# Kernel tuning notes

Measured on AMD Instinct MI355X. Metric: run time of the kernel, lower is better.

The kernel has to match this reference:

```python
import jax, jax.numpy as jnp
import numpy as np

DIM = 512
NUM_EXPERTS = 8
HID = 4 * DIM
B, S = 2, 2048


def setup_inputs() -> dict:
    key = jax.random.key(0)
    ks = jax.random.split(key, 7)
    sc = 0.02
    x = jax.random.normal(ks[0], (B, S, DIM), dtype=jnp.float32)
    Wr = jax.random.normal(ks[1], (DIM, NUM_EXPERTS), dtype=jnp.float32) * sc
    br = jnp.zeros((NUM_EXPERTS,), dtype=jnp.float32)
    W1 = jax.random.normal(ks[2], (NUM_EXPERTS, DIM, HID), dtype=jnp.float32) * sc
    b1 = jnp.zeros((NUM_EXPERTS, HID), dtype=jnp.float32)
    W2 = jax.random.normal(ks[3], (NUM_EXPERTS, HID, DIM), dtype=jnp.float32) * sc
    b2 = jnp.zeros((NUM_EXPERTS, DIM), dtype=jnp.float32)
    return {"x": x, "Wr": Wr, "br": br, "W1": W1, "b1": b1, "W2": W2, "b2": b2}


def reference(x, Wr, br, W1, b1, W2, b2):
    b, s, d = x.shape
    E = Wr.shape[1]
    xf = x.reshape(-1, d)                                   # [N, d]
    N = xf.shape[0]
    logits = xf @ Wr + br                                   # [N, E]
    probs = jax.nn.softmax(logits, axis=-1)
    top_w, top_idx = jax.lax.top_k(probs, 2)                # [N, 2]
    top_w = jax.nn.softmax(top_w, axis=-1)                  # renormalize top-2
    # combine weight per (token, expert); topk indices are distinct so add is safe
    comb = jnp.zeros((N, E), dtype=xf.dtype)
    comb = comb.at[jnp.arange(N)[:, None], top_idx].add(top_w)  # [N, E]
    # dense per-expert MLP (eval mode: dropout is identity); exact GELU as nn.GELU
    h = jax.nn.gelu(jnp.einsum('nd,edf->enf', xf, W1) + b1[:, None, :], approximate=False)
    y = jnp.einsum('enf,efd->end', h, W2) + b2[:, None, :]  # [E, N, d]
    out = jnp.einsum('end,ne->nd', y, comb)                 # weighted combine
    # load-balancing loss
    load = jnp.zeros((E,), dtype=jnp.float32).at[top_idx.reshape(-1)].add(1.0)
    load = load / load.sum()
    lb_loss = jnp.sum((load - 1.0 / E) ** 2)
    return out.reshape(b, s, d), lb_loss, load
```

## Files before the change

### kernel.cpp

```cpp
#include <hip/hip_runtime.h>
#include <hip/hip_bf16.h>

#define DIMD 512
#define NEXP 8
#define HIDN 2048
#define NTOK 4096
#define NASG 8192

typedef short bf16x8 __attribute__((ext_vector_type(8)));
typedef float f32x4 __attribute__((ext_vector_type(4)));

__device__ inline unsigned short f2bf(float f) {
  __hip_bfloat16 h = __float2bfloat16(f);
  return __builtin_bit_cast(unsigned short, h);
}

__device__ inline void gl16(const void* g, void* l) {
  __builtin_amdgcn_global_load_lds(
      (const __attribute__((address_space(1))) unsigned int*)g,
      (__attribute__((address_space(3))) unsigned int*)l, 16, 0, 0);
}

__global__ __launch_bounds__(256) void transpose_both_kernel(
    const float* __restrict__ W1, const float* __restrict__ W2,
    unsigned short* __restrict__ w1t, unsigned short* __restrict__ w2t) {
  __shared__ float tile[64][65];
  int z = blockIdx.z;
  int e = z & 7;
  const float* src; unsigned short* dst; int R, C, r0, c0;
  if (z < 8) { src = W1; dst = w1t; R = DIMD; C = HIDN; c0 = blockIdx.x * 64; r0 = blockIdx.y * 64; }
  else       { src = W2; dst = w2t; R = HIDN; C = DIMD; r0 = blockIdx.x * 64; c0 = blockIdx.y * 64; }
  const float* s = src + (size_t)e * R * C;
  unsigned short* d = dst + (size_t)e * R * C;
  for (int i = threadIdx.x; i < 4096; i += 256) {
    int r = i >> 6, c = i & 63;
    tile[r][c] = s[(size_t)(r0 + r) * C + (c0 + c)];
  }
  __syncthreads();
  for (int i = threadIdx.x; i < 2048; i += 256) {
    int c = i >> 5;
    int r = (i & 31) * 2;
    unsigned lo = f2bf(tile[r][c]);
    unsigned hi = f2bf(tile[r + 1][c]);
    *reinterpret_cast<unsigned*>(d + (size_t)(c0 + c) * R + (r0 + r)) = lo | (hi << 16);
  }
}

__global__ __launch_bounds__(256) void router_kernel(const float* __restrict__ x,
                                                     const float* __restrict__ Wr,
                                                     const float* __restrict__ br,
                                                     int* __restrict__ tidx,
                                                     float* __restrict__ tw,
                                                     unsigned short* __restrict__ xb) {
  int lane = threadIdx.x & 63;
  int n = blockIdx.x * 4 + (threadIdx.x >> 6);
  const float* xr = x + (size_t)n * DIMD;
  unsigned short* xbr = xb + (size_t)n * DIMD;
  float acc[NEXP];
#pragma unroll
  for (int e = 0; e < NEXP; ++e) acc[e] = 0.f;
#pragma unroll
  for (int it = 0; it < 2; ++it) {
    int d0 = it * 256 + lane * 4;
    float4 xv = *reinterpret_cast<const float4*>(xr + d0);
    unsigned p0 = (unsigned)f2bf(xv.x) | ((unsigned)f2bf(xv.y) << 16);
    unsigned p1 = (unsigned)f2bf(xv.z) | ((unsigned)f2bf(xv.w) << 16);
    *reinterpret_cast<uint2*>(xbr + d0) = make_uint2(p0, p1);
    const float* wr = Wr + (size_t)d0 * NEXP;
#pragma unroll
    for (int j = 0; j < 4; ++j) {
      float xj = (&xv.x)[j];
#pragma unroll
      for (int e = 0; e < NEXP; ++e) acc[e] += xj * wr[j * NEXP + e];
    }
  }
#pragma unroll
  for (int e = 0; e < NEXP; ++e) {
    float v = acc[e];
#pragma unroll
    for (int off = 32; off > 0; off >>= 1) v += __shfl_xor(v, off, 64);
    acc[e] = v + br[e];
  }
  if (lane == 0) {
    float m = acc[0];
    for (int e = 1; e < NEXP; ++e) m = fmaxf(m, acc[e]);
    float p[NEXP], s = 0.f;
    for (int e = 0; e < NEXP; ++e) { p[e] = expf(acc[e] - m); s += p[e]; }
    float inv = 1.f / s;
    for (int e = 0; e < NEXP; ++e) p[e] *= inv;
    int i0 = 0; float p0 = p[0];
    for (int e = 1; e < NEXP; ++e) if (p[e] > p0) { p0 = p[e]; i0 = e; }
    int i1 = (i0 == 0) ? 1 : 0; float p1 = p[i1];
    for (int e = 0; e < NEXP; ++e) if (e != i0 && p[e] > p1) { p1 = p[e]; i1 = e; }
    float t = expf(p1 - p0);
    float w0 = 1.f / (1.f + t);
    tidx[2 * n] = i0; tidx[2 * n + 1] = i1;
    tw[2 * n] = w0; tw[2 * n + 1] = t * w0;
  }
}

__global__ __launch_bounds__(1024) void route_pack_kernel(const int* __restrict__ tidx,
                                                          int* __restrict__ off,
                                                          int* __restrict__ list,
                                                          float* __restrict__ out_tail) {
  int tid = threadIdx.x;
  int wv = tid >> 6, lane = tid & 63;

  int ids[8];
#pragma unroll
  for (int j = 0; j < 8; ++j) ids[j] = tidx[tid * 8 + j];

  int c[NEXP];
#pragma unroll
  for (int e = 0; e < NEXP; ++e) c[e] = 0;
#pragma unroll
  for (int j = 0; j < 8; ++j)
#pragma unroll
    for (int e = 0; e < NEXP; ++e) c[e] += (ids[j] == e) ? 1 : 0;

  int inc[NEXP];
#pragma unroll
  for (int e = 0; e < NEXP; ++e) {
    int v = c[e];
#pragma unroll
    for (int d = 1; d < 64; d <<= 1) {
      int t = __shfl_up(v, d, 64);
      if (lane >= d) v += t;
    }
    inc[e] = v;
  }

  __shared__ int wtot[NEXP][16];
  __shared__ int wbase[NEXP][16];
  __shared__ int ebase[NEXP];
  if (lane == 63) {
#pragma unroll
    for (int e = 0; e < NEXP; ++e) wtot[e][wv] = inc[e];
  }
  __syncthreads();
  if (tid == 0) {
    int o = 0;
    float lb = 0.f;
    for (int e = 0; e < NEXP; ++e) {
      int s = 0;
      for (int w = 0; w < 16; ++w) { wbase[e][w] = s; s += wtot[e][w]; }
      ebase[e] = o;
      off[e] = o;
      o += s;
      float l = (float)s / (float)NASG;
      out_tail[1 + e] = l;
      float dd = l - 0.125f;
      lb += dd * dd;
    }
    off[NEXP] = o;
    out_tail[0] = lb;
  }
  __syncthreads();

  int pos[NEXP];
#pragma unroll
  for (int e = 0; e < NEXP; ++e)
    pos[e] = ebase[e] + wbase[e][wv] + (inc[e] - c[e]);

#pragma unroll
  for (int j = 0; j < 8; ++j) {
    int e = ids[j];
    int p = 0;
#pragma unroll
    for (int k = 0; k < NEXP; ++k)
      if (e == k) { p = pos[k]; pos[k] = p + 1; }
    list[p] = tid * 8 + j;
  }
}


__global__ __launch_bounds__(256) void gemm1_kernel(
    const unsigned short* __restrict__ xb,
    const unsigned short* __restrict__ w1t,
    const float* __restrict__ b1,
    const int* __restrict__ off,
    const int* __restrict__ list,
    unsigned short* __restrict__ H) {
  int e = blockIdx.x;
  int offe = off[e];
  int cnt_e = off[e + 1] - offe;
  int n0 = blockIdx.y * 128;
  int m0 = blockIdx.z * 128;
  if (m0 >= cnt_e) return;

  __shared__ char ldsb[36864];

  int tid = threadIdx.x, wv = tid >> 6, lane = tid & 63;
  int rp = lane >> 3, sl = lane & 7;
  int sx = sl ^ rp;
  int rowadd = rp * 2 + (sx >> 2);
  int kq = sx & 3;

  const unsigned short* w1e = w1t + (size_t)e * HIDN * DIMD;
  const unsigned short* asrc[2];
  const unsigned short* bsrc[2];
#pragma unroll
  for (int i = 0; i < 2; ++i) {
    int r = wv * 32 + i * 16 + rowadd;
    int rr = m0 + r;
    int tok = 0;
    if (rr < cnt_e) tok = list[offe + rr] >> 1;
    asrc[i] = xb + (size_t)tok * DIMD + kq * 8;
    bsrc[i] = w1e + (size_t)(n0 + r) * DIMD + kq * 8;
  }
  int dstA0 = wv * 2048;
  int dstA1 = wv * 2048 + 1024;

  f32x4 zero = {0.f, 0.f, 0.f, 0.f};
  f32x4 acc[4][4];
#pragma unroll
  for (int m = 0; m < 4; ++m)
#pragma unroll
    for (int n = 0; n < 4; ++n) acc[m][n] = zero;

  int wave_m = wv >> 1, wave_n = wv & 1;
  int lane16 = lane & 15, kq4 = lane >> 4;
  int ra[4], rb[4];
#pragma unroll
  for (int m = 0; m < 4; ++m) {
    int r = wave_m * 64 + m * 16 + lane16;
    ra[m] = (r >> 1) * 128 + ((((kq4 + (r & 1) * 4)) ^ ((r >> 1) & 7)) << 4);
    int rn = wave_n * 64 + m * 16 + lane16;
    rb[m] = (rn >> 1) * 128 + ((((kq4 + (rn & 1) * 4)) ^ ((rn >> 1) & 7)) << 4);
  }

  const int T = DIMD / 32;
  gl16(asrc[0], ldsb + dstA0);
  gl16(asrc[1], ldsb + dstA1);
  gl16(bsrc[0], ldsb + 8192 + dstA0);
  gl16(bsrc[1], ldsb + 8192 + dstA1);
  __syncthreads();

  for (int t = 0; t < T; ++t) {
    char* cb = ldsb + (t & 1) * 16384;
    if (t + 1 < T) {
      char* nb = ldsb + ((t + 1) & 1) * 16384;
      int k0 = (t + 1) * 32;
      gl16(asrc[0] + k0, nb + dstA0);
      gl16(asrc[1] + k0, nb + dstA1);
      gl16(bsrc[0] + k0, nb + 8192 + dstA0);
      gl16(bsrc[1] + k0, nb + 8192 + dstA1);
    }
    bf16x8 af[4], bfr[4];
#pragma unroll
    for (int m = 0; m < 4; ++m) af[m] = *reinterpret_cast<const bf16x8*>(cb + ra[m]);
#pragma unroll
    for (int n = 0; n < 4; ++n) bfr[n] = *reinterpret_cast<const bf16x8*>(cb + 8192 + rb[n]);
#pragma unroll
    for (int m = 0; m < 4; ++m)
#pragma unroll
      for (int n = 0; n < 4; ++n)
        acc[m][n] = __builtin_amdgcn_mfma_f32_16x16x32_bf16(af[m], bfr[n], acc[m][n], 0, 0, 0);
    __syncthreads();
  }

  unsigned short* Ct = (unsigned short*)ldsb;
  const float* b1e = b1 + e * HIDN;
#pragma unroll
  for (int n = 0; n < 4; ++n) {
    int cl = wave_n * 64 + n * 16 + lane16;
    float bias = b1e[n0 + cl];
#pragma unroll
    for (int m = 0; m < 4; ++m) {
#pragma unroll
      for (int q = 0; q < 4; ++q) {
        int rl = wave_m * 64 + m * 16 + kq4 * 4 + q;
        float v = acc[m][n][q] + bias;
        float g = 0.5f * v * (1.f + erff(v * 0.70710678118654752f));
        Ct[rl * 136 + cl] = f2bf(g);
      }
    }
  }
  __syncthreads();
  for (int u = tid; u < 2048; u += 256) {
    int rl = u >> 4, c8 = (u & 15) * 8;
    int r = m0 + rl;
    if (r < cnt_e) {
      uint4 v = *reinterpret_cast<const uint4*>(Ct + rl * 136 + c8);
      *reinterpret_cast<uint4*>(H + (size_t)(offe + r) * HIDN + n0 + c8) = v;
    }
  }
}

__global__ __launch_bounds__(256) void gemm2_kernel(
    const unsigned short* __restrict__ H,
    const unsigned short* __restrict__ w2t,
    const float* __restrict__ b2,
    const int* __restrict__ off,
    const int* __restrict__ list,
    const float* __restrict__ tw,
    float* __restrict__ Yw) {
  int e = blockIdx.x;
  int offe = off[e];
  int cnt_e = off[e + 1] - offe;
  int n0 = blockIdx.y * 128;
  int m0 = blockIdx.z * 128;
  if (m0 >= cnt_e) return;

  __shared__ char ldsb[32768];

  int tid = threadIdx.x, wv = tid >> 6, lane = tid & 63;
  int rp = lane >> 3, sl = lane & 7;
  int sx = sl ^ rp;
  int rowadd = rp * 2 + (sx >> 2);
  int kq = sx & 3;

  const unsigned short* w2e = w2t + (size_t)e * DIMD * HIDN;
  const unsigned short* asrc[2];
  const unsigned short* bsrc[2];
#pragma unroll
  for (int i = 0; i < 2; ++i) {
    int r = wv * 32 + i * 16 + rowadd;
    int rowa = offe + m0 + r;
    if (rowa > NASG - 1) rowa = NASG - 1;
    asrc[i] = H + (size_t)rowa * HIDN + kq * 8;
    bsrc[i] = w2e + (size_t)(n0 + r) * HIDN + kq * 8;
  }
  int dstA0 = wv * 2048;
  int dstA1 = wv * 2048 + 1024;

  f32x4 zero = {0.f, 0.f, 0.f, 0.f};
  f32x4 acc[4][4];
#pragma unroll
  for (int m = 0; m < 4; ++m)
#pragma unroll
    for (int n = 0; n < 4; ++n) acc[m][n] = zero;

  int wave_m = wv >> 1, wave_n = wv & 1;
  int lane16 = lane & 15, kq4 = lane >> 4;
  int ra[4], rb[4];
#pragma unroll
  for (int m = 0; m < 4; ++m) {
    int r = wave_m * 64 + m * 16 + lane16;
    ra[m] = (r >> 1) * 128 + ((((kq4 + (r & 1) * 4)) ^ ((r >> 1) & 7)) << 4);
    int rn = wave_n * 64 + m * 16 + lane16;
    rb[m] = (rn >> 1) * 128 + ((((kq4 + (rn & 1) * 4)) ^ ((rn >> 1) & 7)) << 4);
  }

  const int T = HIDN / 32;
  gl16(asrc[0], ldsb + dstA0);
  gl16(asrc[1], ldsb + dstA1);
  gl16(bsrc[0], ldsb + 8192 + dstA0);
  gl16(bsrc[1], ldsb + 8192 + dstA1);
  __syncthreads();

  for (int t = 0; t < T; ++t) {
    char* cb = ldsb + (t & 1) * 16384;
    if (t + 1 < T) {
      char* nb = ldsb + ((t + 1) & 1) * 16384;
      int k0 = (t + 1) * 32;
      gl16(asrc[0] + k0, nb + dstA0);
      gl16(asrc[1] + k0, nb + dstA1);
      gl16(bsrc[0] + k0, nb + 8192 + dstA0);
      gl16(bsrc[1] + k0, nb + 8192 + dstA1);
    }
    bf16x8 af[4], bfr[4];
#pragma unroll
    for (int m = 0; m < 4; ++m) af[m] = *reinterpret_cast<const bf16x8*>(cb + ra[m]);
#pragma unroll
    for (int n = 0; n < 4; ++n) bfr[n] = *reinterpret_cast<const bf16x8*>(cb + 8192 + rb[n]);
#pragma unroll
    for (int m = 0; m < 4; ++m)
#pragma unroll
      for (int n = 0; n < 4; ++n)
        acc[m][n] = __builtin_amdgcn_mfma_f32_16x16x32_bf16(af[m], bfr[n], acc[m][n], 0, 0, 0);
    __syncthreads();
  }

  const float* b2e = b2 + e * DIMD;
  float bias[4];
#pragma unroll
  for (int n = 0; n < 4; ++n) bias[n] = b2e[n0 + wave_n * 64 + n * 16 + lane16];
#pragma unroll
  for (int m = 0; m < 4; ++m) {
#pragma unroll
    for (int q = 0; q < 4; ++q) {
      int r = m0 + wave_m * 64 + m * 16 + kq4 * 4 + q;
      if (r < cnt_e) {
        int a = list[offe + r];
        float w = tw[a];
        float* yrow = Yw + (size_t)a * DIMD;
#pragma unroll
        for (int n = 0; n < 4; ++n) {
          int col = n0 + wave_n * 64 + n * 16 + lane16;
          yrow[col] = w * (acc[m][n][q] + bias[n]);
        }
      }
    }
  }
}

__global__ __launch_bounds__(256) void combine_kernel(const float* __restrict__ Yw,
                                                      float* __restrict__ out) {
  int i = (blockIdx.x * 256 + threadIdx.x) * 4;
  int n = i >> 9;
  int d = i & 511;
  float4 a = *reinterpret_cast<const float4*>(Yw + (size_t)(2 * n) * DIMD + d);
  float4 b = *reinterpret_cast<const float4*>(Yw + (size_t)(2 * n + 1) * DIMD + d);
  float4 o;
  o.x = a.x + b.x; o.y = a.y + b.y; o.z = a.z + b.z; o.w = a.w + b.w;
  *reinterpret_cast<float4*>(out + i) = o;
}

extern "C" void kernel_launch(void* const* d_in, const int* in_sizes, int n_in,
                              void* d_out, int out_size, void* d_ws, size_t ws_size,
                              hipStream_t stream) {
  const float* x  = (const float*)d_in[0];
  const float* Wr = (const float*)d_in[1];
  const float* br = (const float*)d_in[2];
  const float* W1 = (const float*)d_in[3];
  const float* b1 = (const float*)d_in[4];
  const float* W2 = (const float*)d_in[5];
  const float* b2 = (const float*)d_in[6];
  float* out = (float*)d_out;

  char* ws = (char*)d_ws;
  unsigned short* xb  = (unsigned short*)ws;  ws += (size_t)NTOK * DIMD * 2;
  unsigned short* w1t = (unsigned short*)ws;  ws += (size_t)NEXP * HIDN * DIMD * 2;
  unsigned short* w2t = (unsigned short*)ws;  ws += (size_t)NEXP * DIMD * HIDN * 2;
  unsigned short* H   = (unsigned short*)ws;  ws += (size_t)NASG * HIDN * 2;
  float* Yw = (float*)ws;                     ws += (size_t)NASG * DIMD * 4;
  float* tw = (float*)ws;                     ws += (size_t)NASG * 4;
  int* tidx = (int*)ws;                       ws += (size_t)NASG * 4;
  int* list = (int*)ws;                       ws += (size_t)NASG * 4;
  int* offp = (int*)ws;

  transpose_both_kernel<<<dim3(32, 8, 16), 256, 0, stream>>>(W1, W2, w1t, w2t);
  router_kernel<<<NTOK / 4, 256, 0, stream>>>(x, Wr, br, tidx, tw, xb);
  route_pack_kernel<<<1, 1024, 0, stream>>>(tidx, offp, list, out + (size_t)NTOK * DIMD);
  gemm1_kernel<<<dim3(NEXP, HIDN / 128, NASG / 128), 256, 0, stream>>>(xb, w1t, b1, offp, list, H);
  gemm2_kernel<<<dim3(NEXP, DIMD / 128, NASG / 128), 256, 0, stream>>>(H, w2t, b2, offp, list, tw, Yw);
  combine_kernel<<<2048, 256, 0, stream>>>(Yw, out);
}
```

Before: 118.5 us.

## Keep two global-to-LDS loads in flight with vmcnt-gated barriers in expert GEMMs

Both expert GEMM main loops are rewritten so two K-stages are prefetched before the loop starts. Each iteration waits only for the older stage (s_waitcnt vmcnt(4)) before its barrier, instead of draining all memory ops through __syncthreads. The next stage is issued into the buffer just consumed, after a post-compute barrier, so one load stays outstanding during each compute step. This aims to hide global load latency better, at the cost of an extra barrier per iteration and reliance on hand-placed waitcnt and sched_barrier ordering.

```diff
diff --git a/kernel.cpp b/kernel.cpp
--- a/kernel.cpp
+++ b/kernel.cpp
@@ -20,6 +20,19 @@
       (const __attribute__((address_space(1))) unsigned int*)g,
       (__attribute__((address_space(3))) unsigned int*)l, 16, 0, 0);
 }
+
+#define PIPE_WAIT4_BAR() do { \
+  asm volatile("s_waitcnt vmcnt(4)" ::: "memory"); \
+  __builtin_amdgcn_s_barrier(); \
+  __builtin_amdgcn_sched_barrier(0); } while (0)
+#define PIPE_WAIT0_BAR() do { \
+  asm volatile("s_waitcnt vmcnt(0)" ::: "memory"); \
+  __builtin_amdgcn_s_barrier(); \
+  __builtin_amdgcn_sched_barrier(0); } while (0)
+#define PIPE_POST_BAR() do { \
+  asm volatile("" ::: "memory"); \
+  __builtin_amdgcn_sched_barrier(0); \
+  __builtin_amdgcn_s_barrier(); } while (0)
 
 __global__ __launch_bounds__(256) void transpose_both_kernel(
     const float* __restrict__ W1, const float* __restrict__ W2,
@@ -229,23 +242,13 @@
     rb[m] = (rn >> 1) * 128 + ((((kq4 + (rn & 1) * 4)) ^ ((rn >> 1) & 7)) << 4);
   }
 
-  const int T = DIMD / 32;
-  gl16(asrc[0], ldsb + dstA0);
-  gl16(asrc[1], ldsb + dstA1);
-  gl16(bsrc[0], ldsb + 8192 + dstA0);
-  gl16(bsrc[1], ldsb + 8192 + dstA1);
-  __syncthreads();
-
-  for (int t = 0; t < T; ++t) {
-    char* cb = ldsb + (t & 1) * 16384;
-    if (t + 1 < T) {
-      char* nb = ldsb + ((t + 1) & 1) * 16384;
-      int k0 = (t + 1) * 32;
-      gl16(asrc[0] + k0, nb + dstA0);
-      gl16(asrc[1] + k0, nb + dstA1);
-      gl16(bsrc[0] + k0, nb + 8192 + dstA0);
-      gl16(bsrc[1] + k0, nb + 8192 + dstA1);
-    }
+  auto stage = [&](char* nb, int k0) {
+    gl16(asrc[0] + k0, nb + dstA0);
+    gl16(asrc[1] + k0, nb + dstA1);
+    gl16(bsrc[0] + k0, nb + 8192 + dstA0);
+    gl16(bsrc[1] + k0, nb + 8192 + dstA1);
+  };
+  auto compute = [&](const char* cb) {
     bf16x8 af[4], bfr[4];
 #pragma unroll
     for (int m = 0; m < 4; ++m) af[m] = *reinterpret_cast<const bf16x8*>(cb + ra[m]);
@@ -256,8 +259,24 @@
 #pragma unroll
       for (int n = 0; n < 4; ++n)
         acc[m][n] = __builtin_amdgcn_mfma_f32_16x16x32_bf16(af[m], bfr[n], acc[m][n], 0, 0, 0);
-    __syncthreads();
-  }
+  };
+
+  const int T = DIMD / 32;
+  stage(ldsb, 0);
+  stage(ldsb + 16384, 32);
+  for (int t = 0; t < T - 2; ++t) {
+    char* cb = ldsb + (t & 1) * 16384;
+    PIPE_WAIT4_BAR();
+    compute(cb);
+    PIPE_POST_BAR();
+    stage(cb, (t + 2) * 32);
+  }
+  PIPE_WAIT4_BAR();
+  compute(ldsb + ((T - 2) & 1) * 16384);
+  PIPE_POST_BAR();
+  PIPE_WAIT0_BAR();
+  compute(ldsb + ((T - 1) & 1) * 16384);
+  PIPE_POST_BAR();
 
   unsigned short* Ct = (unsigned short*)ldsb;
   const float* b1e = b1 + e * HIDN;
@@ -342,23 +361,13 @@
     rb[m] = (rn >> 1) * 128 + ((((kq4 + (rn & 1) * 4)) ^ ((rn >> 1) & 7)) << 4);
   }
 
-  const int T = HIDN / 32;
-  gl16(asrc[0], ldsb + dstA0);
-  gl16(asrc[1], ldsb + dstA1);
-  gl16(bsrc[0], ldsb + 8192 + dstA0);
-  gl16(bsrc[1], ldsb + 8192 + dstA1);
-  __syncthreads();
-
-  for (int t = 0; t < T; ++t) {
-    char* cb = ldsb + (t & 1) * 16384;
-    if (t + 1 < T) {
-      char* nb = ldsb + ((t + 1) & 1) * 16384;
-      int k0 = (t + 1) * 32;
-      gl16(asrc[0] + k0, nb + dstA0);
-      gl16(asrc[1] + k0, nb + dstA1);
-      gl16(bsrc[0] + k0, nb + 8192 + dstA0);
-      gl16(bsrc[1] + k0, nb + 8192 + dstA1);
-    }
+  auto stage = [&](char* nb, int k0) {
+    gl16(asrc[0] + k0, nb + dstA0);
+    gl16(asrc[1] + k0, nb + dstA1);
+    gl16(bsrc[0] + k0, nb + 8192 + dstA0);
+    gl16(bsrc[1] + k0, nb + 8192 + dstA1);
+  };
+  auto compute = [&](const char* cb) {
     bf16x8 af[4], bfr[4];
 #pragma unroll
     for (int m = 0; m < 4; ++m) af[m] = *reinterpret_cast<const bf16x8*>(cb + ra[m]);
@@ -369,8 +378,24 @@
 #pragma unroll
       for (int n = 0; n < 4; ++n)
         acc[m][n] = __builtin_amdgcn_mfma_f32_16x16x32_bf16(af[m], bfr[n], acc[m][n], 0, 0, 0);
-    __syncthreads();
-  }
+  };
+
+  const int T = HIDN / 32;
+  stage(ldsb, 0);
+  stage(ldsb + 16384, 32);
+  for (int t = 0; t < T - 2; ++t) {
+    char* cb = ldsb + (t & 1) * 16384;
+    PIPE_WAIT4_BAR();
+    compute(cb);
+    PIPE_POST_BAR();
+    stage(cb, (t + 2) * 32);
+  }
+  PIPE_WAIT4_BAR();
+  compute(ldsb + ((T - 2) & 1) * 16384);
+  PIPE_POST_BAR();
+  PIPE_WAIT0_BAR();
+  compute(ldsb + ((T - 1) & 1) * 16384);
+  PIPE_POST_BAR();
 
   const float* b2e = b2 + e * DIMD;
   float bias[4];
```

After: 118.3 us. Within noise of the previous version (-0.2%).
